# Performance work log

Hardware: AMD Instinct MI355X
Metric: run time of the kernel (lower is better)

## Reference

```python
import jax, jax.numpy as jnp
import numpy as np

H = 64; W = 64; P = 16; NPH = 4; NPW = 4; PH = 16; PW = 16; ZD = 32; HD = 1024; UD = 3; B = 256


def affine_grid(theta, Ho, Wo):
    # torch F.affine_grid, align_corners=False. theta [N,2,3] -> grid [N,Ho,Wo,2]
    xs = (2.0 * jnp.arange(Wo, dtype=theta.dtype) + 1.0) / Wo - 1.0
    ys = (2.0 * jnp.arange(Ho, dtype=theta.dtype) + 1.0) / Ho - 1.0
    X, Y = jnp.meshgrid(xs, ys)  # [Ho,Wo] each, x varies along last axis
    base = jnp.stack([X, Y, jnp.ones_like(X)], axis=-1)  # [Ho,Wo,3]
    return jnp.einsum('nij,hwj->nhwi', theta, base)


def grid_sample(img, grid):
    # torch F.grid_sample bilinear, padding_mode='zeros', align_corners=False
    # img [N,H,W], grid [N,Ho,Wo,2] in [-1,1]
    Hi, Wi = img.shape[1], img.shape[2]
    x = (grid[..., 0] + 1.0) * Wi / 2.0 - 0.5
    y = (grid[..., 1] + 1.0) * Hi / 2.0 - 0.5
    x0 = jnp.floor(x); y0 = jnp.floor(y)
    wx = x - x0; wy = y - y0

    def gather(ix, iy):
        valid = (ix >= 0) & (ix < Wi) & (iy >= 0) & (iy < Hi)
        ixc = jnp.clip(ix, 0, Wi - 1).astype(jnp.int32)
        iyc = jnp.clip(iy, 0, Hi - 1).astype(jnp.int32)
        v = jax.vmap(lambda im, yy, xx: im[yy, xx])(img, iyc, ixc)
        return jnp.where(valid, v, 0.0)

    return (gather(x0, y0) * (1 - wx) * (1 - wy)
            + gather(x0 + 1, y0) * wx * (1 - wy)
            + gather(x0, y0 + 1) * (1 - wx) * wy
            + gather(x0 + 1, y0 + 1) * wx * wy)


def rot_tr(u):
    # rotTrMatrix: u [N,3] (angle, tx, ty) -> [N,2,3]
    c = jnp.cos(u[:, 0]); s = jnp.sin(u[:, 0])
    R = jnp.stack([jnp.stack([c, -s], -1), jnp.stack([s, c], -1)], -2)  # [N,2,2]
    return jnp.concatenate([R, u[:, 1:3, None]], axis=2)


def anchor_theta():
    # anchor_move: identity rotation + per-part grid-cell-center translations
    tx = (np.arange(NPW) * (W / NPW) + W / NPW / 2) / W - 0.5
    ty = (np.arange(NPH) * (H / NPH) + H / NPH / 2) / H - 0.5
    th = np.tile(np.concatenate([np.eye(2), np.zeros((2, 1))], axis=1)[None], (P, 1, 1)).astype(np.float32)
    for k in range(P):
        th[k, 0, 2] = tx[k % NPW]
        th[k, 1, 2] = ty[k // NPW]
    return jnp.asarray(th)


def forward(inputs, W1, b1, W2, b2, Wum, bum, Wuv, buv, Wgm, bgm, Wgv, bgv, Wz, M, eps_u, eps_g):
    hid = jax.nn.relu(inputs.reshape(-1, H * W) @ W1 + b1)
    hid = jax.nn.relu(hid @ W2 + b2)
    # global transform distribution (note: F.threshold(x,-6,6) -> 6 where x<=-6)
    gmu = jnp.tanh(hid @ Wgm + bgm)
    gpre = hid @ Wgv + bgv
    gvar = jnp.exp(jnp.where(gpre > -6.0, gpre, 6.0))
    gu = gmu + gvar * eps_g  # sample_u uses mu + var*eps (var, not std) as in source
    # per-part transform distribution (F.threshold(x,-6,-6) -> clamp below at -6)
    umu = jnp.tanh(hid @ Wum + bum)
    upre = hid @ Wuv + buv
    uvar = jnp.exp(jnp.where(upre > -6.0, upre, -6.0))
    u = (umu + uvar * eps_u).reshape(-1, UD)  # [B*P,3]
    # decode parts (input is ones, as in source)
    parts = jax.nn.sigmoid(jnp.ones((B, ZD), inputs.dtype) @ Wz).reshape(B * P, PH, PW)
    padh = (H - PH) // 2; padw = (W - PW) // 2
    parts = jnp.pad(parts, ((0, 0), (padh, H - PH - padh), (padw, W - PW - padw)))
    # anchor placement of parts and kernel masks
    th_a = jnp.tile(anchor_theta(), (B, 1, 1))  # [B*P,2,3], part-minor ordering
    g_a = affine_grid(th_a, H, W)
    parts = grid_sample(parts, g_a)                     # [B*P,H,W]
    KM = grid_sample(M[:B * P].reshape(B * P, H, W), g_a)
    # per-part rotation+translation for parts; translation-only for kernel
    theta = rot_tr(u)                                   # [B*P,2,3]
    g = affine_grid(theta, H, W)
    eye = jnp.broadcast_to(jnp.eye(2, dtype=theta.dtype), (B * P, 2, 2))
    theta_K = jnp.concatenate([eye, theta[:, :, 2:3]], axis=2)
    g_K = affine_grid(theta_K, H, W)
    KM = grid_sample(KM, g_K).reshape(B, P, H, W)
    xp = grid_sample(parts, g).reshape(B, P, H, W)
    # masked weighted compositing
    num = jnp.sum(xp * KM, axis=1)
    den = jnp.sum(KM, axis=1)
    den = jnp.where(den == 0.0, 1.0, den)
    x = num / den
    # global transform
    theta_g = rot_tr(gu)
    g_g = affine_grid(theta_g, H, W)
    return grid_sample(x, g_g)[:, None]  # [B,1,H,W]


def setup_inputs() -> dict:
    key = jax.random.key(0)
    ks = jax.random.split(key, 18)

    def lin(k, fin, fout):
        return jax.random.normal(k, (fin, fout), jnp.float32) / np.sqrt(fin)

    return {
        'inputs': jax.random.uniform(ks[0], (B, H * W), jnp.float32),
        'W1': lin(ks[1], H * W, HD), 'b1': jnp.zeros((HD,), jnp.float32),
        'W2': lin(ks[2], HD, HD), 'b2': jnp.zeros((HD,), jnp.float32),
        'Wum': lin(ks[3], HD, P * UD), 'bum': jnp.zeros((P * UD,), jnp.float32),
        'Wuv': lin(ks[4], HD, P * UD), 'buv': jnp.zeros((P * UD,), jnp.float32),
        'Wgm': lin(ks[5], HD, UD), 'bgm': jnp.zeros((UD,), jnp.float32),
        'Wgv': lin(ks[6], HD, UD), 'bgv': jnp.zeros((UD,), jnp.float32),
        'Wz': lin(ks[7], ZD, P * PH * PW),
        'M': jax.random.uniform(ks[8], (B * P, 1, H, W), jnp.float32),
        'eps_u': jax.random.normal(ks[9], (B, P * UD), jnp.float32),
        'eps_g': jax.random.normal(ks[10], (B, UD), jnp.float32),
    }


def reference(inputs, W1, b1, W2, b2, Wum, bum, Wuv, buv, Wgm, bgm, Wgv, bgv, Wz, M, eps_u, eps_g):
    return forward(inputs, W1, b1, W2, b2, Wum, bum, Wuv, buv, Wgm, bgm, Wgv, bgv, Wz, M, eps_u, eps_g)
```

## Files before the change

kernel.cpp:

```cpp
#include <hip/hip_runtime.h>
#include <math.h>

#define SPLITK 8

typedef __bf16 bf16x8 __attribute__((ext_vector_type(8)));
typedef float  f32x4  __attribute__((ext_vector_type(4)));

__device__ inline unsigned short bf16rne(float x) {
    unsigned int u = __float_as_uint(x);
    unsigned int r = u + 0x7FFFu + ((u >> 16) & 1u);
    return (unsigned short)(r >> 16);
}
__device__ inline float bf16tof(unsigned short h) {
    return __uint_as_float(((unsigned int)h) << 16);
}

__global__ __launch_bounds__(256) void prep_all(
    const float* __restrict__ inputs,
    const float* __restrict__ W1, const float* __restrict__ W2,
    const float* __restrict__ Wum, const float* __restrict__ Wuv,
    const float* __restrict__ Wgm, const float* __restrict__ Wgv,
    const float* __restrict__ Wz,
    unsigned short* __restrict__ Ahi, unsigned short* __restrict__ Alo,
    unsigned short* __restrict__ W1Thi, unsigned short* __restrict__ W1Tlo,
    unsigned short* __restrict__ W2Thi, unsigned short* __restrict__ W2Tlo,
    float* __restrict__ WT, float* __restrict__ partsb)
{
    __shared__ float t[32][33];
    int bid = blockIdx.x;
    int tid = threadIdx.x;
    if (bid < 4096 || (bid >= 8192 && bid < 9216)) {
        const float* W = (bid < 4096) ? W1 : W2;
        unsigned short* Thi = (bid < 4096) ? W1Thi : W2Thi;
        unsigned short* Tlo = (bid < 4096) ? W1Tlo : W2Tlo;
        int K = (bid < 4096) ? 4096 : 1024;
        int b2 = (bid < 4096) ? bid : (bid - 8192);
        int n0 = (b2 & 31) * 32, k0 = (b2 >> 5) * 32;
        int c = tid & 31, r0 = tid >> 5;
#pragma unroll
        for (int i = 0; i < 4; i++)
            t[r0 + 8 * i][c] = W[(size_t)(k0 + r0 + 8 * i) * 1024 + n0 + c];
        __syncthreads();
        int kk = tid & 31, n1 = tid >> 5;
#pragma unroll
        for (int i = 0; i < 4; i++) {
            float x = t[kk][n1 + 8 * i];
            unsigned short h = bf16rne(x);
            unsigned short l = bf16rne(x - bf16tof(h));
            size_t o = (size_t)(n0 + n1 + 8 * i) * K + k0 + kk;
            Thi[o] = h;
            Tlo[o] = l;
        }
    } else if (bid < 8192) {
        int id = (bid - 4096) * 256 + tid;
        float x = inputs[id];
        unsigned short h = bf16rne(x);
        Ahi[id] = h;
        Alo[id] = bf16rne(x - bf16tof(h));
    } else if (bid < 9624) {
        int id = (bid - 9216) * 256 + tid;
        int o = id >> 10;
        int k = id & 1023;
        float v;
        if (o < 48)       v = Wum[k * 48 + o];
        else if (o < 96)  v = Wuv[k * 48 + (o - 48)];
        else if (o < 99)  v = Wgm[k * 3 + (o - 96)];
        else              v = Wgv[k * 3 + (o - 99)];
        WT[id] = v;
    } else {
        int idx = (bid - 9624) * 256 + tid;
        float s = 0.f;
#pragma unroll
        for (int z = 0; z < 32; z++) s += Wz[z * 4096 + idx];
        partsb[idx] = 1.f / (1.f + expf(-s));
    }
}

__global__ __launch_bounds__(256) void gemm_bf16x3(
    const unsigned short* __restrict__ Ahi, const unsigned short* __restrict__ Alo,
    const unsigned short* __restrict__ Bhi, const unsigned short* __restrict__ Blo,
    float* __restrict__ psum, int K, int kchunk)
{
    __shared__ unsigned short Ah[4096], Al[4096], Bh[4096], Bl[4096];
    int tid = threadIdx.x;
    int n0 = blockIdx.x * 64, m0 = blockIdx.y * 64;
    int kb = blockIdx.z * kchunk;
    int wid = tid >> 6, lane = tid & 63;
    int wm = wid & 1, wn = wid >> 1;
    int lm = lane & 15, q = lane >> 4;

    int r0 = tid >> 3, ch0 = tid & 7;
    int r1 = (tid + 256) >> 3, ch1 = (tid + 256) & 7;
    int l0 = r0 * 64 + 8 * (ch0 ^ (r0 & 7));
    int l1 = r1 * 64 + 8 * (ch1 ^ (r1 & 7));
    size_t ga0 = (size_t)(m0 + r0) * K + kb + ch0 * 8;
    size_t ga1 = (size_t)(m0 + r1) * K + kb + ch1 * 8;
    size_t gb0 = (size_t)(n0 + r0) * K + kb + ch0 * 8;
    size_t gb1 = (size_t)(n0 + r1) * K + kb + ch1 * 8;

    f32x4 acc[2][2] = {};

    int nkt = kchunk >> 6;
    uint4 vah0, vah1, val0, val1, vbh0, vbh1, vbl0, vbl1;
    vah0 = *(const uint4*)(Ahi + ga0);
    vah1 = *(const uint4*)(Ahi + ga1);
    val0 = *(const uint4*)(Alo + ga0);
    val1 = *(const uint4*)(Alo + ga1);
    vbh0 = *(const uint4*)(Bhi + gb0);
    vbh1 = *(const uint4*)(Bhi + gb1);
    vbl0 = *(const uint4*)(Blo + gb0);
    vbl1 = *(const uint4*)(Blo + gb1);

    int frm0 = (wm * 32 + lm) * 64;
    int frm1 = (wm * 32 + 16 + lm) * 64;
    int frn0 = (wn * 32 + lm) * 64;
    int frn1 = (wn * 32 + 16 + lm) * 64;
    int sw = lm & 7;

    for (int kt = 0; kt < nkt; kt++) {
        __syncthreads();
        *(uint4*)(Ah + l0) = vah0;
        *(uint4*)(Ah + l1) = vah1;
        *(uint4*)(Al + l0) = val0;
        *(uint4*)(Al + l1) = val1;
        *(uint4*)(Bh + l0) = vbh0;
        *(uint4*)(Bh + l1) = vbh1;
        *(uint4*)(Bl + l0) = vbl0;
        *(uint4*)(Bl + l1) = vbl1;
        __syncthreads();
        if (kt + 1 < nkt) {
            size_t o = (size_t)(kt + 1) * 64;
            vah0 = *(const uint4*)(Ahi + ga0 + o);
            vah1 = *(const uint4*)(Ahi + ga1 + o);
            val0 = *(const uint4*)(Alo + ga0 + o);
            val1 = *(const uint4*)(Alo + ga1 + o);
            vbh0 = *(const uint4*)(Bhi + gb0 + o);
            vbh1 = *(const uint4*)(Bhi + gb1 + o);
            vbl0 = *(const uint4*)(Blo + gb0 + o);
            vbl1 = *(const uint4*)(Blo + gb1 + o);
        }
#pragma unroll
        for (int ks = 0; ks < 2; ks++) {
            int cidx = 8 * (((ks << 2) + q) ^ sw);
            bf16x8 ah0 = *(const bf16x8*)(Ah + frm0 + cidx);
            bf16x8 ah1 = *(const bf16x8*)(Ah + frm1 + cidx);
            bf16x8 al0 = *(const bf16x8*)(Al + frm0 + cidx);
            bf16x8 al1 = *(const bf16x8*)(Al + frm1 + cidx);
            bf16x8 bh0 = *(const bf16x8*)(Bh + frn0 + cidx);
            bf16x8 bh1 = *(const bf16x8*)(Bh + frn1 + cidx);
            bf16x8 bl0 = *(const bf16x8*)(Bl + frn0 + cidx);
            bf16x8 bl1 = *(const bf16x8*)(Bl + frn1 + cidx);
            acc[0][0] = __builtin_amdgcn_mfma_f32_16x16x32_bf16(ah0, bh0, acc[0][0], 0, 0, 0);
            acc[0][0] = __builtin_amdgcn_mfma_f32_16x16x32_bf16(ah0, bl0, acc[0][0], 0, 0, 0);
            acc[0][0] = __builtin_amdgcn_mfma_f32_16x16x32_bf16(al0, bh0, acc[0][0], 0, 0, 0);
            acc[0][1] = __builtin_amdgcn_mfma_f32_16x16x32_bf16(ah0, bh1, acc[0][1], 0, 0, 0);
            acc[0][1] = __builtin_amdgcn_mfma_f32_16x16x32_bf16(ah0, bl1, acc[0][1], 0, 0, 0);
            acc[0][1] = __builtin_amdgcn_mfma_f32_16x16x32_bf16(al0, bh1, acc[0][1], 0, 0, 0);
            acc[1][0] = __builtin_amdgcn_mfma_f32_16x16x32_bf16(ah1, bh0, acc[1][0], 0, 0, 0);
            acc[1][0] = __builtin_amdgcn_mfma_f32_16x16x32_bf16(ah1, bl0, acc[1][0], 0, 0, 0);
            acc[1][0] = __builtin_amdgcn_mfma_f32_16x16x32_bf16(al1, bh0, acc[1][0], 0, 0, 0);
            acc[1][1] = __builtin_amdgcn_mfma_f32_16x16x32_bf16(ah1, bh1, acc[1][1], 0, 0, 0);
            acc[1][1] = __builtin_amdgcn_mfma_f32_16x16x32_bf16(ah1, bl1, acc[1][1], 0, 0, 0);
            acc[1][1] = __builtin_amdgcn_mfma_f32_16x16x32_bf16(al1, bh1, acc[1][1], 0, 0, 0);
        }
    }

    float* op = psum + (size_t)blockIdx.z * (256 * 1024);
#pragma unroll
    for (int mt = 0; mt < 2; mt++)
#pragma unroll
        for (int nt = 0; nt < 2; nt++) {
            int row = m0 + wm * 32 + mt * 16 + q * 4;
            int col = n0 + wn * 32 + nt * 16 + lm;
#pragma unroll
            for (int r = 0; r < 4; r++)
                op[(size_t)(row + r) * 1024 + col] = acc[mt][nt][r];
        }
}

__global__ __launch_bounds__(256) void reduce_bias_relu_split(
    const float* __restrict__ psum, const float* __restrict__ bias,
    unsigned short* __restrict__ hi, unsigned short* __restrict__ lo)
{
    int i = blockIdx.x * 256 + threadIdx.x;
    float v = 0.f;
#pragma unroll
    for (int s = 0; s < SPLITK; s++) v += psum[(size_t)s * 262144 + i];
    v += bias[i & 1023];
    v = fmaxf(v, 0.f);
    unsigned short h = bf16rne(v);
    hi[i] = h;
    lo[i] = bf16rne(v - bf16tof(h));
}

__global__ __launch_bounds__(512) void heads_v3(
    const float* __restrict__ psum, const float* __restrict__ b2,
    const float* __restrict__ WT,
    const float* __restrict__ bum, const float* __restrict__ buv,
    const float* __restrict__ bgm, const float* __restrict__ bgv,
    const float* __restrict__ eps_u, const float* __restrict__ eps_g,
    float* __restrict__ u_out, float* __restrict__ gu_out)
{
    int b = blockIdx.x;
    int tid = threadIdx.x;
    int w = tid >> 6, l = tid & 63;

    float4 hr[4];
#pragma unroll
    for (int i = 0; i < 4; i++) {
        int k = b * 1024 + i * 256 + l * 4;
        float4 acc = *(const float4*)(psum + k);
#pragma unroll
        for (int s = 1; s < SPLITK; s++) {
            float4 t = *(const float4*)(psum + (size_t)s * 262144 + k);
            acc.x += t.x; acc.y += t.y; acc.z += t.z; acc.w += t.w;
        }
        float4 bb = *(const float4*)(b2 + i * 256 + l * 4);
        acc.x = fmaxf(acc.x + bb.x, 0.f);
        acc.y = fmaxf(acc.y + bb.y, 0.f);
        acc.z = fmaxf(acc.z + bb.z, 0.f);
        acc.w = fmaxf(acc.w + bb.w, 0.f);
        hr[i] = acc;
    }

    int o = w;
    int rm = (o < 48) ? o : (48 + o);
    int rv = (o < 48) ? (o + 48) : (51 + o);
    float4 wm[4], wv[4];
    {
        const float* wp = WT + rm * 1024 + l * 4;
#pragma unroll
        for (int i = 0; i < 4; i++) wm[i] = *(const float4*)(wp + i * 256);
        wp = WT + rv * 1024 + l * 4;
#pragma unroll
        for (int i = 0; i < 4; i++) wv[i] = *(const float4*)(wp + i * 256);
    }

    while (o < 51) {
        int onext = o + 8;
        float4 wmn[4], wvn[4];
        if (onext < 51) {
            int rm2 = (onext < 48) ? onext : (48 + onext);
            int rv2 = (onext < 48) ? (onext + 48) : (51 + onext);
            const float* wp = WT + rm2 * 1024 + l * 4;
#pragma unroll
            for (int i = 0; i < 4; i++) wmn[i] = *(const float4*)(wp + i * 256);
            wp = WT + rv2 * 1024 + l * 4;
#pragma unroll
            for (int i = 0; i < 4; i++) wvn[i] = *(const float4*)(wp + i * 256);
        }
        float am = 0.f, av = 0.f;
#pragma unroll
        for (int i = 0; i < 4; i++) {
            am = fmaf(hr[i].x, wm[i].x, am);
            am = fmaf(hr[i].y, wm[i].y, am);
            am = fmaf(hr[i].z, wm[i].z, am);
            am = fmaf(hr[i].w, wm[i].w, am);
            av = fmaf(hr[i].x, wv[i].x, av);
            av = fmaf(hr[i].y, wv[i].y, av);
            av = fmaf(hr[i].z, wv[i].z, av);
            av = fmaf(hr[i].w, wv[i].w, av);
        }
#pragma unroll
        for (int s = 32; s; s >>= 1) {
            am += __shfl_xor(am, s, 64);
            av += __shfl_xor(av, s, 64);
        }
        if (l == 0) {
            if (o < 48) {
                float umu = tanhf(am + bum[o]);
                float uvar = expf(fmaxf(av + buv[o], -6.f));
                u_out[b * 48 + o] = umu + uvar * eps_u[b * 48 + o];
            } else {
                int n = o - 48;
                float gmu = tanhf(am + bgm[n]);
                float gpre = av + bgv[n];
                float gvar = expf(gpre > -6.f ? gpre : 6.f);
                gu_out[b * 3 + n] = gmu + gvar * eps_g[b * 3 + n];
            }
        }
#pragma unroll
        for (int i = 0; i < 4; i++) { wm[i] = wmn[i]; wv[i] = wvn[i]; }
        o = onext;
    }
}

__global__ __launch_bounds__(256) void composite_v6b(
    const float* __restrict__ M, const float* __restrict__ parts,
    const float* __restrict__ u, float* __restrict__ xout)
{
    __shared__ float patch[4096];
    __shared__ float plane[2][17 * 64];
    __shared__ float pc[16], psn[16], ptx[16], pty[16];
    int b = blockIdx.x >> 2;
    int quarter = blockIdx.x & 3;
    int tid = threadIdx.x;
    int brow0 = quarter * 16;

    for (int i = tid; i < 4096; i += 256) patch[i] = parts[i];
    if (tid < 16) {
        const float* up = u + (b * 16 + tid) * 3;
        float ang = up[0];
        pc[tid] = cosf(ang);
        psn[tid] = sinf(ang);
        ptx[tid] = up[1];
        pty[tid] = up[2];
    }
    __syncthreads();

    int j = tid & 63;
    int i0 = brow0 + (tid >> 6) * 4;
    float xnv = (float)(2 * j + 1) * (1.f / 64.f) - 1.f;

    float num[4] = {}, den[4] = {};
    const float* Mb = M + ((size_t)(b * 16) << 12);

    auto calc_iy = [&](int p, int& iy, int& iY, float& wy) {
        int dy = 8 * (p >> 2) - 12;
        float ay = fminf(fmaxf(32.f * pty[p], -16384.f), 16384.f);
        float fay = floorf(ay);
        wy = ay - fay;
        iy = (int)fay;
        iY = iy + dy;
    };

    int rr0 = tid >> 4, c0 = tid & 15;
    int rr1 = (tid + 256) >> 4, c1 = (tid + 256) & 15;

    int iy_arr[17], iY_arr[17]; float wy_arr[17];
#pragma unroll
    for (int p = 0; p < 16; p++) calc_iy(p, iy_arr[p], iY_arr[p], wy_arr[p]);

    float4 pfA0, pfA1;
    {
        int lo = brow0 + iY_arr[0];
        pfA0 = *(const float4*)(Mb + (min(max(lo + rr0, 0), 63) << 6) + c0 * 4);
        if (tid < 16)
            pfA1 = *(const float4*)(Mb + (min(max(lo + rr1, 0), 63) << 6) + c1 * 4);
        float4* dst = (float4*)plane[0];
        dst[tid] = pfA0;
        if (tid < 16) dst[tid + 256] = pfA1;
    }
    {
        int lo = brow0 + iY_arr[1];
        const float* Mp = Mb + (1 << 12);
        pfA0 = *(const float4*)(Mp + (min(max(lo + rr0, 0), 63) << 6) + c0 * 4);
        if (tid < 16)
            pfA1 = *(const float4*)(Mp + (min(max(lo + rr1, 0), 63) << 6) + c1 * 4);
    }
    __syncthreads();

    for (int p = 0; p < 16; p++) {
        int cur = p & 1;
        if (p + 1 < 16) {
            float4* dst = (float4*)plane[1 - cur];
            dst[tid] = pfA0;
            if (tid < 16) dst[tid + 256] = pfA1;
        }
        if (p + 2 < 16) {
            int lo = brow0 + iY_arr[p + 2];
            const float* Mp = Mb + ((size_t)(p + 2) << 12);
            pfA0 = *(const float4*)(Mp + (min(max(lo + rr0, 0), 63) << 6) + c0 * 4);
            if (tid < 16)
                pfA1 = *(const float4*)(Mp + (min(max(lo + rr1, 0), 63) << 6) + c1 * 4);
        }

        int iy = iy_arr[p], iY = iY_arr[p];
        float wy = wy_arr[p];
        int dx = 8 * (p & 3) - 12;
        int dy = 8 * (p >> 2) - 12;
        float c = pc[p], s = psn[p], tx = ptx[p];

        float ax = fminf(fmaxf(32.f * tx, -16384.f), 16384.f);
        float fax = floorf(ax);
        float wx = ax - fax;
        int ix = (int)fax;

        int x0 = j + ix;
        int X = x0 + dx;
        bool vc0 = ((unsigned)x0 < 64u) && ((unsigned)X < 64u);
        bool vc1 = ((unsigned)(x0 + 1) < 64u) && ((unsigned)(X + 1) < 64u);
        float w0 = vc0 ? (1.f - wx) : 0.f;
        float w1 = vc1 ? wx : 0.f;
        int Xc0 = min(max(X, 0), 63);
        int Xc1 = min(max(X + 1, 0), 63);

        const float* pl = plane[cur];
        float R[5];
#pragma unroll
        for (int r = 0; r < 5; r++) {
            int i = i0 + r;
            bool vr = ((unsigned)(i + iy) < 64u) && ((unsigned)(i + iY) < 64u);
            int lrow = (tid >> 6) * 4 + r;
            const float* row = pl + (lrow << 6);
            float val = fmaf(w0, row[Xc0], w1 * row[Xc1]);
            R[r] = vr ? val : 0.f;
        }

        float Ax = fmaf(c, xnv, tx);
        float Ay = fmaf(s, xnv, pty[p]);
        int ox = 24 - dx, oy = 24 - dy;
        float oxf = (float)ox, oyf = (float)oy;
        const float* pp = patch + (p << 8);
#pragma unroll
        for (int r = 0; r < 4; r++) {
            int i = i0 + r;
            float km = fmaf(wy, R[r + 1] - R[r], R[r]);
            den[r] += km;

            float ynv = (float)(2 * i + 1) * (1.f / 64.f) - 1.f;
            float gx = fmaf(-s, ynv, Ax);
            float gy = fmaf(c, ynv, Ay);
            float xs = fmaf(gx, 32.f, 31.5f);
            float ysv = fmaf(gy, 32.f, 31.5f);
            if (xs >= oxf - 1.f && xs < oxf + 16.f &&
                ysv >= oyf - 1.f && ysv < oyf + 16.f) {
                float xf = floorf(xs), yf = floorf(ysv);
                float wxx = xs - xf, wyy = ysv - yf;
                int a0 = (int)yf - oy;
                int b0c = (int)xf - ox;
                float v00 = 0.f, v10 = 0.f, v01 = 0.f, v11 = 0.f;
                if ((unsigned)a0 < 16u) {
                    const float* pr = pp + a0 * 16;
                    if ((unsigned)b0c < 16u) v00 = pr[b0c];
                    if ((unsigned)(b0c + 1) < 16u) v10 = pr[b0c + 1];
                }
                if ((unsigned)(a0 + 1) < 16u) {
                    const float* pr = pp + (a0 + 1) * 16;
                    if ((unsigned)b0c < 16u) v01 = pr[b0c];
                    if ((unsigned)(b0c + 1) < 16u) v11 = pr[b0c + 1];
                }
                float top = fmaf(wxx, v10 - v00, v00);
                float bot = fmaf(wxx, v11 - v01, v01);
                float xp = fmaf(wyy, bot - top, top);
                num[r] = fmaf(xp, km, num[r]);
            }
        }
        __syncthreads();
    }

    float* xo = xout + ((size_t)b << 12);
#pragma unroll
    for (int r = 0; r < 4; r++) {
        float d = (den[r] == 0.f) ? 1.f : den[r];
        xo[(i0 + r) * 64 + j] = num[r] / d;
    }
}

__global__ __launch_bounds__(256) void final_kernel(
    const float* __restrict__ xin, const float* __restrict__ gu,
    float* __restrict__ out)
{
    int id = blockIdx.x * 256 + threadIdx.x;
    int b = id >> 12;
    int pix = id & 4095;
    int ii = pix >> 6, jj = pix & 63;
    float ang = gu[b * 3 + 0], tx = gu[b * 3 + 1], ty = gu[b * 3 + 2];
    float c = cosf(ang), s = sinf(ang);
    float xn = (float)(2 * jj + 1) * (1.f / 64.f) - 1.f;
    float yn = (float)(2 * ii + 1) * (1.f / 64.f) - 1.f;
    float gx = c * xn - s * yn + tx;
    float gy = s * xn + c * yn + ty;
    float xs = (gx + 1.f) * 32.f - 0.5f;
    float ysv = (gy + 1.f) * 32.f - 0.5f;
    float xf = floorf(xs), yf = floorf(ysv);
    float wx = xs - xf, wy = ysv - yf;
    int x0 = (int)xf, y0 = (int)yf;
    const float* xp = xin + ((size_t)b << 12);
    float v00 = 0.f, v10 = 0.f, v01 = 0.f, v11 = 0.f;
    bool vx0 = (unsigned)x0 < 64u, vx1 = (unsigned)(x0 + 1) < 64u;
    if ((unsigned)y0 < 64u) {
        if (vx0) v00 = xp[y0 * 64 + x0];
        if (vx1) v10 = xp[y0 * 64 + x0 + 1];
    }
    if ((unsigned)(y0 + 1) < 64u) {
        if (vx0) v01 = xp[(y0 + 1) * 64 + x0];
        if (vx1) v11 = xp[(y0 + 1) * 64 + x0 + 1];
    }
    out[id] = v00 * (1.f - wx) * (1.f - wy) + v10 * wx * (1.f - wy)
            + v01 * (1.f - wx) * wy + v11 * wx * wy;
}

extern "C" void kernel_launch(void* const* d_in, const int* in_sizes, int n_in,
                              void* d_out, int out_size, void* d_ws, size_t ws_size,
                              hipStream_t stream)
{
    (void)in_sizes; (void)n_in; (void)out_size; (void)ws_size;
    const float* inputs = (const float*)d_in[0];
    const float* W1  = (const float*)d_in[1];
    const float* b1  = (const float*)d_in[2];
    const float* W2  = (const float*)d_in[3];
    const float* b2  = (const float*)d_in[4];
    const float* Wum = (const float*)d_in[5];
    const float* bum = (const float*)d_in[6];
    const float* Wuv = (const float*)d_in[7];
    const float* buv = (const float*)d_in[8];
    const float* Wgm = (const float*)d_in[9];
    const float* bgm = (const float*)d_in[10];
    const float* Wgv = (const float*)d_in[11];
    const float* bgv = (const float*)d_in[12];
    const float* Wz  = (const float*)d_in[13];
    const float* Mm  = (const float*)d_in[14];
    const float* eps_u = (const float*)d_in[15];
    const float* eps_g = (const float*)d_in[16];

    float* ws = (float*)d_ws;
    float* psum      = ws;
    float* x_buf     = ws + 2097152;
    float* u_buf     = ws + 3145728;
    float* gu_buf    = ws + 3158016;
    float* parts_buf = ws + 3158784;
    float* WTh_buf   = ws + 3162880;
    unsigned short* us = (unsigned short*)(ws + 3267328);
    unsigned short* Ahi   = us;
    unsigned short* Alo   = Ahi + 1048576;
    unsigned short* W1Thi = Alo + 1048576;
    unsigned short* W1Tlo = W1Thi + 4194304;
    unsigned short* W2Thi = W1Tlo + 4194304;
    unsigned short* W2Tlo = W2Thi + 1048576;
    unsigned short* H1hi  = W2Tlo + 1048576;
    unsigned short* H1lo  = H1hi + 262144;

    prep_all<<<9640, 256, 0, stream>>>(inputs, W1, W2, Wum, Wuv, Wgm, Wgv, Wz,
                                       Ahi, Alo, W1Thi, W1Tlo, W2Thi, W2Tlo,
                                       WTh_buf, parts_buf);

    gemm_bf16x3<<<dim3(16, 4, SPLITK), 256, 0, stream>>>(Ahi, Alo, W1Thi, W1Tlo,
                                                         psum, 4096, 4096 / SPLITK);
    reduce_bias_relu_split<<<1024, 256, 0, stream>>>(psum, b1, H1hi, H1lo);
    gemm_bf16x3<<<dim3(16, 4, SPLITK), 256, 0, stream>>>(H1hi, H1lo, W2Thi, W2Tlo,
                                                         psum, 1024, 1024 / SPLITK);
    heads_v3<<<256, 512, 0, stream>>>(psum, b2, WTh_buf, bum, buv, bgm, bgv,
                                      eps_u, eps_g, u_buf, gu_buf);
    composite_v6b<<<1024, 256, 0, stream>>>(Mm, parts_buf, u_buf, x_buf);
    final_kernel<<<4096, 256, 0, stream>>>(x_buf, gu_buf, (float*)d_out);
}
```

Before: 207.7 us.

## Fuse split-K reduction into GEMM1 and composite with final warp

The first GEMM now uses a per-tile atomic counter, so the last split-K block for each tile sums the partials and applies bias, ReLU and the bf16 hi/lo split. This removes the separate reduction kernel. The composite and final grid-sample kernels are merged into one 1024-thread block per batch image, which loads whole 64x64 M planes into shared memory and warps the composited image from shared memory instead of going through a global buffer. The trade-off is fewer blocks (256) with larger shared-memory use, plus a threadfence/atomic serialization tail in the GEMM.

```diff
diff --git a/kernel.cpp b/kernel.cpp
--- a/kernel.cpp
+++ b/kernel.cpp
@@ -24,7 +24,7 @@
     unsigned short* __restrict__ Ahi, unsigned short* __restrict__ Alo,
     unsigned short* __restrict__ W1Thi, unsigned short* __restrict__ W1Tlo,
     unsigned short* __restrict__ W2Thi, unsigned short* __restrict__ W2Tlo,
-    float* __restrict__ WT, float* __restrict__ partsb)
+    float* __restrict__ WT, float* __restrict__ partsb, int* __restrict__ ctr)
 {
     __shared__ float t[32][33];
     int bid = blockIdx.x;
@@ -73,15 +73,20 @@
 #pragma unroll
         for (int z = 0; z < 32; z++) s += Wz[z * 4096 + idx];
         partsb[idx] = 1.f / (1.f + expf(-s));
-    }
-}
-
-__global__ __launch_bounds__(256) void gemm_bf16x3(
+        if (bid == 9639 && tid < 64) ctr[tid] = 0;
+    }
+}
+
+__global__ __launch_bounds__(256) void gemm_bf16x3_l1(
     const unsigned short* __restrict__ Ahi, const unsigned short* __restrict__ Alo,
     const unsigned short* __restrict__ Bhi, const unsigned short* __restrict__ Blo,
-    float* __restrict__ psum, int K, int kchunk)
+    float* __restrict__ psum, const float* __restrict__ b1,
+    unsigned short* __restrict__ H1hi, unsigned short* __restrict__ H1lo,
+    int* __restrict__ ctr)
 {
+    const int K = 4096, kchunk = 512;
     __shared__ unsigned short Ah[4096], Al[4096], Bh[4096], Bl[4096];
+    __shared__ int lastFlag;
     int tid = threadIdx.x;
     int n0 = blockIdx.x * 64, m0 = blockIdx.y * 64;
     int kb = blockIdx.z * kchunk;
@@ -176,21 +181,138 @@
             for (int r = 0; r < 4; r++)
                 op[(size_t)(row + r) * 1024 + col] = acc[mt][nt][r];
         }
-}
-
-__global__ __launch_bounds__(256) void reduce_bias_relu_split(
-    const float* __restrict__ psum, const float* __restrict__ bias,
-    unsigned short* __restrict__ hi, unsigned short* __restrict__ lo)
+
+    __syncthreads();
+    if (tid == 0) {
+        __threadfence();
+        int old = atomicAdd(&ctr[blockIdx.y * 16 + blockIdx.x], 1);
+        lastFlag = (old == SPLITK - 1);
+    }
+    __syncthreads();
+    if (!lastFlag) return;
+    __threadfence();
+
+#pragma unroll
+    for (int mt = 0; mt < 2; mt++)
+#pragma unroll
+        for (int nt = 0; nt < 2; nt++) {
+            int row = m0 + wm * 32 + mt * 16 + q * 4;
+            int col = n0 + wn * 32 + nt * 16 + lm;
+#pragma unroll
+            for (int r = 0; r < 4; r++) {
+                size_t e = (size_t)(row + r) * 1024 + col;
+                float v = 0.f;
+#pragma unroll
+                for (int s = 0; s < SPLITK; s++) v += psum[(size_t)s * 262144 + e];
+                v += b1[col];
+                v = fmaxf(v, 0.f);
+                unsigned short h = bf16rne(v);
+                H1hi[e] = h;
+                H1lo[e] = bf16rne(v - bf16tof(h));
+            }
+        }
+}
+
+__global__ __launch_bounds__(256) void gemm_bf16x3(
+    const unsigned short* __restrict__ Ahi, const unsigned short* __restrict__ Alo,
+    const unsigned short* __restrict__ Bhi, const unsigned short* __restrict__ Blo,
+    float* __restrict__ psum, int K, int kchunk)
 {
-    int i = blockIdx.x * 256 + threadIdx.x;
-    float v = 0.f;
-#pragma unroll
-    for (int s = 0; s < SPLITK; s++) v += psum[(size_t)s * 262144 + i];
-    v += bias[i & 1023];
-    v = fmaxf(v, 0.f);
-    unsigned short h = bf16rne(v);
-    hi[i] = h;
-    lo[i] = bf16rne(v - bf16tof(h));
+    __shared__ unsigned short Ah[4096], Al[4096], Bh[4096], Bl[4096];
+    int tid = threadIdx.x;
+    int n0 = blockIdx.x * 64, m0 = blockIdx.y * 64;
+    int kb = blockIdx.z * kchunk;
+    int wid = tid >> 6, lane = tid & 63;
+    int wm = wid & 1, wn = wid >> 1;
+    int lm = lane & 15, q = lane >> 4;
+
+    int r0 = tid >> 3, ch0 = tid & 7;
+    int r1 = (tid + 256) >> 3, ch1 = (tid + 256) & 7;
+    int l0 = r0 * 64 + 8 * (ch0 ^ (r0 & 7));
+    int l1 = r1 * 64 + 8 * (ch1 ^ (r1 & 7));
+    size_t ga0 = (size_t)(m0 + r0) * K + kb + ch0 * 8;
+    size_t ga1 = (size_t)(m0 + r1) * K + kb + ch1 * 8;
+    size_t gb0 = (size_t)(n0 + r0) * K + kb + ch0 * 8;
+    size_t gb1 = (size_t)(n0 + r1) * K + kb + ch1 * 8;
+
+    f32x4 acc[2][2] = {};
+
+    int nkt = kchunk >> 6;
+    uint4 vah0, vah1, val0, val1, vbh0, vbh1, vbl0, vbl1;
+    vah0 = *(const uint4*)(Ahi + ga0);
+    vah1 = *(const uint4*)(Ahi + ga1);
+    val0 = *(const uint4*)(Alo + ga0);
+    val1 = *(const uint4*)(Alo + ga1);
+    vbh0 = *(const uint4*)(Bhi + gb0);
+    vbh1 = *(const uint4*)(Bhi + gb1);
+    vbl0 = *(const uint4*)(Blo + gb0);
+    vbl1 = *(const uint4*)(Blo + gb1);
+
+    int frm0 = (wm * 32 + lm) * 64;
+    int frm1 = (wm * 32 + 16 + lm) * 64;
+    int frn0 = (wn * 32 + lm) * 64;
+    int frn1 = (wn * 32 + 16 + lm) * 64;
+    int sw = lm & 7;
+
+    for (int kt = 0; kt < nkt; kt++) {
+        __syncthreads();
+        *(uint4*)(Ah + l0) = vah0;
+        *(uint4*)(Ah + l1) = vah1;
+        *(uint4*)(Al + l0) = val0;
+        *(uint4*)(Al + l1) = val1;
+        *(uint4*)(Bh + l0) = vbh0;
+        *(uint4*)(Bh + l1) = vbh1;
+        *(uint4*)(Bl + l0) = vbl0;
+        *(uint4*)(Bl + l1) = vbl1;
+        __syncthreads();
+        if (kt + 1 < nkt) {
+            size_t o = (size_t)(kt + 1) * 64;
+            vah0 = *(const uint4*)(Ahi + ga0 + o);
+            vah1 = *(const uint4*)(Ahi + ga1 + o);
+            val0 = *(const uint4*)(Alo + ga0 + o);
+            val1 = *(const uint4*)(Alo + ga1 + o);
+            vbh0 = *(const uint4*)(Bhi + gb0 + o);
+            vbh1 = *(const uint4*)(Bhi + gb1 + o);
+            vbl0 = *(const uint4*)(Blo + gb0 + o);
+            vbl1 = *(const uint4*)(Blo + gb1 + o);
+        }
+#pragma unroll
+        for (int ks = 0; ks < 2; ks++) {
+            int cidx = 8 * (((ks << 2) + q) ^ sw);
+            bf16x8 ah0 = *(const bf16x8*)(Ah + frm0 + cidx);
+            bf16x8 ah1 = *(const bf16x8*)(Ah + frm1 + cidx);
+            bf16x8 al0 = *(const bf16x8*)(Al + frm0 + cidx);
+            bf16x8 al1 = *(const bf16x8*)(Al + frm1 + cidx);
+            bf16x8 bh0 = *(const bf16x8*)(Bh + frn0 + cidx);
+            bf16x8 bh1 = *(const bf16x8*)(Bh + frn1 + cidx);
+            bf16x8 bl0 = *(const bf16x8*)(Bl + frn0 + cidx);
+            bf16x8 bl1 = *(const bf16x8*)(Bl + frn1 + cidx);
+            acc[0][0] = __builtin_amdgcn_mfma_f32_16x16x32_bf16(ah0, bh0, acc[0][0], 0, 0, 0);
+            acc[0][0] = __builtin_amdgcn_mfma_f32_16x16x32_bf16(ah0, bl0, acc[0][0], 0, 0, 0);
+            acc[0][0] = __builtin_amdgcn_mfma_f32_16x16x32_bf16(al0, bh0, acc[0][0], 0, 0, 0);
+            acc[0][1] = __builtin_amdgcn_mfma_f32_16x16x32_bf16(ah0, bh1, acc[0][1], 0, 0, 0);
+            acc[0][1] = __builtin_amdgcn_mfma_f32_16x16x32_bf16(ah0, bl1, acc[0][1], 0, 0, 0);
+            acc[0][1] = __builtin_amdgcn_mfma_f32_16x16x32_bf16(al0, bh1, acc[0][1], 0, 0, 0);
+            acc[1][0] = __builtin_amdgcn_mfma_f32_16x16x32_bf16(ah1, bh0, acc[1][0], 0, 0, 0);
+            acc[1][0] = __builtin_amdgcn_mfma_f32_16x16x32_bf16(ah1, bl0, acc[1][0], 0, 0, 0);
+            acc[1][0] = __builtin_amdgcn_mfma_f32_16x16x32_bf16(al1, bh0, acc[1][0], 0, 0, 0);
+            acc[1][1] = __builtin_amdgcn_mfma_f32_16x16x32_bf16(ah1, bh1, acc[1][1], 0, 0, 0);
+            acc[1][1] = __builtin_amdgcn_mfma_f32_16x16x32_bf16(ah1, bl1, acc[1][1], 0, 0, 0);
+            acc[1][1] = __builtin_amdgcn_mfma_f32_16x16x32_bf16(al1, bh1, acc[1][1], 0, 0, 0);
+        }
+    }
+
+    float* op = psum + (size_t)blockIdx.z * (256 * 1024);
+#pragma unroll
+    for (int mt = 0; mt < 2; mt++)
+#pragma unroll
+        for (int nt = 0; nt < 2; nt++) {
+            int row = m0 + wm * 32 + mt * 16 + q * 4;
+            int col = n0 + wn * 32 + nt * 16 + lm;
+#pragma unroll
+            for (int r = 0; r < 4; r++)
+                op[(size_t)(row + r) * 1024 + col] = acc[mt][nt][r];
+        }
 }
 
 __global__ __launch_bounds__(512) void heads_v3(
@@ -285,19 +407,18 @@
     }
 }
 
-__global__ __launch_bounds__(256) void composite_v6b(
+__global__ __launch_bounds__(1024) void composite_final(
     const float* __restrict__ M, const float* __restrict__ parts,
-    const float* __restrict__ u, float* __restrict__ xout)
+    const float* __restrict__ u, const float* __restrict__ gu,
+    float* __restrict__ out)
 {
     __shared__ float patch[4096];
-    __shared__ float plane[2][17 * 64];
+    __shared__ float plane[2][4096];
     __shared__ float pc[16], psn[16], ptx[16], pty[16];
-    int b = blockIdx.x >> 2;
-    int quarter = blockIdx.x & 3;
+    int b = blockIdx.x;
     int tid = threadIdx.x;
-    int brow0 = quarter * 16;
-
-    for (int i = tid; i < 4096; i += 256) patch[i] = parts[i];
+
+    for (int i = tid; i < 4096; i += 1024) patch[i] = parts[i];
     if (tid < 16) {
         const float* up = u + (b * 16 + tid) * 3;
         float ang = up[0];
@@ -306,75 +427,36 @@
         ptx[tid] = up[1];
         pty[tid] = up[2];
     }
+
+    const float* Mb = M + ((size_t)(b * 16) << 12);
+    ((float4*)plane[0])[tid] = ((const float4*)Mb)[tid];
+    float4 pfn = ((const float4*)(Mb + 4096))[tid];
     __syncthreads();
 
     int j = tid & 63;
-    int i0 = brow0 + (tid >> 6) * 4;
+    int i0 = (tid >> 6) * 4;
     float xnv = (float)(2 * j + 1) * (1.f / 64.f) - 1.f;
 
     float num[4] = {}, den[4] = {};
-    const float* Mb = M + ((size_t)(b * 16) << 12);
-
-    auto calc_iy = [&](int p, int& iy, int& iY, float& wy) {
-        int dy = 8 * (p >> 2) - 12;
-        float ay = fminf(fmaxf(32.f * pty[p], -16384.f), 16384.f);
-        float fay = floorf(ay);
-        wy = ay - fay;
-        iy = (int)fay;
-        iY = iy + dy;
-    };
-
-    int rr0 = tid >> 4, c0 = tid & 15;
-    int rr1 = (tid + 256) >> 4, c1 = (tid + 256) & 15;
-
-    int iy_arr[17], iY_arr[17]; float wy_arr[17];
-#pragma unroll
-    for (int p = 0; p < 16; p++) calc_iy(p, iy_arr[p], iY_arr[p], wy_arr[p]);
-
-    float4 pfA0, pfA1;
-    {
-        int lo = brow0 + iY_arr[0];
-        pfA0 = *(const float4*)(Mb + (min(max(lo + rr0, 0), 63) << 6) + c0 * 4);
-        if (tid < 16)
-            pfA1 = *(const float4*)(Mb + (min(max(lo + rr1, 0), 63) << 6) + c1 * 4);
-        float4* dst = (float4*)plane[0];
-        dst[tid] = pfA0;
-        if (tid < 16) dst[tid + 256] = pfA1;
-    }
-    {
-        int lo = brow0 + iY_arr[1];
-        const float* Mp = Mb + (1 << 12);
-        pfA0 = *(const float4*)(Mp + (min(max(lo + rr0, 0), 63) << 6) + c0 * 4);
-        if (tid < 16)
-            pfA1 = *(const float4*)(Mp + (min(max(lo + rr1, 0), 63) << 6) + c1 * 4);
-    }
-    __syncthreads();
 
     for (int p = 0; p < 16; p++) {
         int cur = p & 1;
-        if (p + 1 < 16) {
-            float4* dst = (float4*)plane[1 - cur];
-            dst[tid] = pfA0;
-            if (tid < 16) dst[tid + 256] = pfA1;
-        }
-        if (p + 2 < 16) {
-            int lo = brow0 + iY_arr[p + 2];
-            const float* Mp = Mb + ((size_t)(p + 2) << 12);
-            pfA0 = *(const float4*)(Mp + (min(max(lo + rr0, 0), 63) << 6) + c0 * 4);
-            if (tid < 16)
-                pfA1 = *(const float4*)(Mp + (min(max(lo + rr1, 0), 63) << 6) + c1 * 4);
-        }
-
-        int iy = iy_arr[p], iY = iY_arr[p];
-        float wy = wy_arr[p];
+        if (p + 1 < 16) ((float4*)plane[1 - cur])[tid] = pfn;
+        if (p + 2 < 16) pfn = ((const float4*)(Mb + ((size_t)(p + 2) << 12)))[tid];
+
         int dx = 8 * (p & 3) - 12;
         int dy = 8 * (p >> 2) - 12;
-        float c = pc[p], s = psn[p], tx = ptx[p];
+        float c = pc[p], s = psn[p], tx = ptx[p], ty = pty[p];
 
         float ax = fminf(fmaxf(32.f * tx, -16384.f), 16384.f);
         float fax = floorf(ax);
         float wx = ax - fax;
         int ix = (int)fax;
+        float ay = fminf(fmaxf(32.f * ty, -16384.f), 16384.f);
+        float fay = floorf(ay);
+        float wy = ay - fay;
+        int iy = (int)fay;
+        int iY = iy + dy;
 
         int x0 = j + ix;
         int X = x0 + dx;
@@ -390,15 +472,16 @@
 #pragma unroll
         for (int r = 0; r < 5; r++) {
             int i = i0 + r;
-            bool vr = ((unsigned)(i + iy) < 64u) && ((unsigned)(i + iY) < 64u);
-            int lrow = (tid >> 6) * 4 + r;
-            const float* row = pl + (lrow << 6);
+            int ri = i + iY;
+            bool vr = ((unsigned)(i + iy) < 64u) && ((unsigned)ri < 64u);
+            int ric = min(max(ri, 0), 63);
+            const float* row = pl + (ric << 6);
             float val = fmaf(w0, row[Xc0], w1 * row[Xc1]);
             R[r] = vr ? val : 0.f;
         }
 
         float Ax = fmaf(c, xnv, tx);
-        float Ay = fmaf(s, xnv, pty[p]);
+        float Ay = fmaf(s, xnv, ty);
         int ox = 24 - dx, oy = 24 - dy;
         float oxf = (float)ox, oyf = (float)oy;
         const float* pp = patch + (p << 8);
@@ -439,46 +522,46 @@
         __syncthreads();
     }
 
-    float* xo = xout + ((size_t)b << 12);
+    float* xl = plane[0];
 #pragma unroll
     for (int r = 0; r < 4; r++) {
         float d = (den[r] == 0.f) ? 1.f : den[r];
-        xo[(i0 + r) * 64 + j] = num[r] / d;
-    }
-}
-
-__global__ __launch_bounds__(256) void final_kernel(
-    const float* __restrict__ xin, const float* __restrict__ gu,
-    float* __restrict__ out)
-{
-    int id = blockIdx.x * 256 + threadIdx.x;
-    int b = id >> 12;
-    int pix = id & 4095;
-    int ii = pix >> 6, jj = pix & 63;
-    float ang = gu[b * 3 + 0], tx = gu[b * 3 + 1], ty = gu[b * 3 + 2];
-    float c = cosf(ang), s = sinf(ang);
-    float xn = (float)(2 * jj + 1) * (1.f / 64.f) - 1.f;
-    float yn = (float)(2 * ii + 1) * (1.f / 64.f) - 1.f;
-    float gx = c * xn - s * yn + tx;
-    float gy = s * xn + c * yn + ty;
-    float xs = (gx + 1.f) * 32.f - 0.5f;
-    float ysv = (gy + 1.f) * 32.f - 0.5f;
-    float xf = floorf(xs), yf = floorf(ysv);
-    float wx = xs - xf, wy = ysv - yf;
-    int x0 = (int)xf, y0 = (int)yf;
-    const float* xp = xin + ((size_t)b << 12);
-    float v00 = 0.f, v10 = 0.f, v01 = 0.f, v11 = 0.f;
-    bool vx0 = (unsigned)x0 < 64u, vx1 = (unsigned)(x0 + 1) < 64u;
-    if ((unsigned)y0 < 64u) {
-        if (vx0) v00 = xp[y0 * 64 + x0];
-        if (vx1) v10 = xp[y0 * 64 + x0 + 1];
-    }
-    if ((unsigned)(y0 + 1) < 64u) {
-        if (vx0) v01 = xp[(y0 + 1) * 64 + x0];
-        if (vx1) v11 = xp[(y0 + 1) * 64 + x0 + 1];
-    }
-    out[id] = v00 * (1.f - wx) * (1.f - wy) + v10 * wx * (1.f - wy)
-            + v01 * (1.f - wx) * wy + v11 * wx * wy;
+        xl[(i0 + r) * 64 + j] = num[r] / d;
+    }
+    __syncthreads();
+
+    float ang = gu[b * 3 + 0], gtx = gu[b * 3 + 1], gty = gu[b * 3 + 2];
+    float cg = cosf(ang), sg = sinf(ang);
+    float* ob = out + ((size_t)b << 12);
+#pragma unroll
+    for (int r = 0; r < 4; r++) {
+        int i = i0 + r;
+        float ynv = (float)(2 * i + 1) * (1.f / 64.f) - 1.f;
+        float gx = cg * xnv - sg * ynv + gtx;
+        float gy = sg * xnv + cg * ynv + gty;
+        gx = fminf(fmaxf(gx, -8.f), 8.f);
+        gy = fminf(fmaxf(gy, -8.f), 8.f);
+        float xs = fmaf(gx, 32.f, 31.5f);
+        float ysv = fmaf(gy, 32.f, 31.5f);
+        float xf = floorf(xs), yf = floorf(ysv);
+        float wx = xs - xf, wy = ysv - yf;
+        int x0 = (int)xf, y0 = (int)yf;
+        float v00 = 0.f, v10 = 0.f, v01 = 0.f, v11 = 0.f;
+        bool vx0 = (unsigned)x0 < 64u, vx1 = (unsigned)(x0 + 1) < 64u;
+        if ((unsigned)y0 < 64u) {
+            const float* row = xl + y0 * 64;
+            if (vx0) v00 = row[x0];
+            if (vx1) v10 = row[x0 + 1];
+        }
+        if ((unsigned)(y0 + 1) < 64u) {
+            const float* row = xl + (y0 + 1) * 64;
+            if (vx0) v01 = row[x0];
+            if (vx1) v11 = row[x0 + 1];
+        }
+        float top = fmaf(wx, v10 - v00, v00);
+        float bot = fmaf(wx, v11 - v01, v01);
+        ob[i * 64 + j] = fmaf(wy, bot - top, top);
+    }
 }
 
 extern "C" void kernel_launch(void* const* d_in, const int* in_sizes, int n_in,
@@ -506,12 +589,12 @@
 
     float* ws = (float*)d_ws;
     float* psum      = ws;
-    float* x_buf     = ws + 2097152;
-    float* u_buf     = ws + 3145728;
-    float* gu_buf    = ws + 3158016;
-    float* parts_buf = ws + 3158784;
-    float* WTh_buf   = ws + 3162880;
-    unsigned short* us = (unsigned short*)(ws + 3267328);
+    float* u_buf     = ws + 2097152;
+    float* gu_buf    = u_buf + 12288;
+    float* parts_buf = gu_buf + 768;
+    float* WTh_buf   = parts_buf + 4096;
+    int*   ctr       = (int*)(WTh_buf + 104448);
+    unsigned short* us = (unsigned short*)(ctr + 64);
     unsigned short* Ahi   = us;
     unsigned short* Alo   = Ahi + 1048576;
     unsigned short* W1Thi = Alo + 1048576;
@@ -523,15 +606,14 @@
 
     prep_all<<<9640, 256, 0, stream>>>(inputs, W1, W2, Wum, Wuv, Wgm, Wgv, Wz,
                                        Ahi, Alo, W1Thi, W1Tlo, W2Thi, W2Tlo,
-                                       WTh_buf, parts_buf);
-
-    gemm_bf16x3<<<dim3(16, 4, SPLITK), 256, 0, stream>>>(Ahi, Alo, W1Thi, W1Tlo,
-                                                         psum, 4096, 4096 / SPLITK);
-    reduce_bias_relu_split<<<1024, 256, 0, stream>>>(psum, b1, H1hi, H1lo);
+                                       WTh_buf, parts_buf, ctr);
+
+    gemm_bf16x3_l1<<<dim3(16, 4, SPLITK), 256, 0, stream>>>(
+        Ahi, Alo, W1Thi, W1Tlo, psum, b1, H1hi, H1lo, ctr);
     gemm_bf16x3<<<dim3(16, 4, SPLITK), 256, 0, stream>>>(H1hi, H1lo, W2Thi, W2Tlo,
                                                          psum, 1024, 1024 / SPLITK);
     heads_v3<<<256, 512, 0, stream>>>(psum, b2, WTh_buf, bum, buv, bgm, bgv,
                                       eps_u, eps_g, u_buf, gu_buf);
-    composite_v6b<<<1024, 256, 0, stream>>>(Mm, parts_buf, u_buf, x_buf);
-    final_kernel<<<4096, 256, 0, stream>>>(x_buf, gu_buf, (float*)d_out);
-}
+    composite_final<<<256, 1024, 0, stream>>>(Mm, parts_buf, u_buf, gu_buf,
+                                              (float*)d_out);
+}
```

New measurement: 221.7 us. 6.8% more time.

## Fuse composite and final grid-sample into one per-image 1024-thread kernel

Applied to the files above, without the earlier changes.

Merges the compositing kernel and the final affine grid_sample kernel. One 1024-thread block now handles a whole image, keeps the composited image in shared memory and samples it there, which removes the global round trip of x_buf and one launch. Each block now stages full 64x64 mask planes instead of shifted 17-row windows, and rows are clamped at read time. The trade is fewer blocks (256 instead of 1024), which lowers parallelism on a large GPU, and more shared memory per block. It also adds a clamp on grid coordinates.

```diff
diff --git a/kernel.cpp b/kernel.cpp
--- a/kernel.cpp
+++ b/kernel.cpp
@@ -285,19 +285,18 @@
     }
 }
 
-__global__ __launch_bounds__(256) void composite_v6b(
+__global__ __launch_bounds__(1024) void composite_final(
     const float* __restrict__ M, const float* __restrict__ parts,
-    const float* __restrict__ u, float* __restrict__ xout)
+    const float* __restrict__ u, const float* __restrict__ gu,
+    float* __restrict__ out)
 {
     __shared__ float patch[4096];
-    __shared__ float plane[2][17 * 64];
+    __shared__ float plane[2][4096];
     __shared__ float pc[16], psn[16], ptx[16], pty[16];
-    int b = blockIdx.x >> 2;
-    int quarter = blockIdx.x & 3;
+    int b = blockIdx.x;
     int tid = threadIdx.x;
-    int brow0 = quarter * 16;
-
-    for (int i = tid; i < 4096; i += 256) patch[i] = parts[i];
+
+    for (int i = tid; i < 4096; i += 1024) patch[i] = parts[i];
     if (tid < 16) {
         const float* up = u + (b * 16 + tid) * 3;
         float ang = up[0];
@@ -306,75 +305,36 @@
         ptx[tid] = up[1];
         pty[tid] = up[2];
     }
+
+    const float* Mb = M + ((size_t)(b * 16) << 12);
+    ((float4*)plane[0])[tid] = ((const float4*)Mb)[tid];
+    float4 pfn = ((const float4*)(Mb + 4096))[tid];
     __syncthreads();
 
     int j = tid & 63;
-    int i0 = brow0 + (tid >> 6) * 4;
+    int i0 = (tid >> 6) * 4;
     float xnv = (float)(2 * j + 1) * (1.f / 64.f) - 1.f;
 
     float num[4] = {}, den[4] = {};
-    const float* Mb = M + ((size_t)(b * 16) << 12);
-
-    auto calc_iy = [&](int p, int& iy, int& iY, float& wy) {
-        int dy = 8 * (p >> 2) - 12;
-        float ay = fminf(fmaxf(32.f * pty[p], -16384.f), 16384.f);
-        float fay = floorf(ay);
-        wy = ay - fay;
-        iy = (int)fay;
-        iY = iy + dy;
-    };
-
-    int rr0 = tid >> 4, c0 = tid & 15;
-    int rr1 = (tid + 256) >> 4, c1 = (tid + 256) & 15;
-
-    int iy_arr[17], iY_arr[17]; float wy_arr[17];
-#pragma unroll
-    for (int p = 0; p < 16; p++) calc_iy(p, iy_arr[p], iY_arr[p], wy_arr[p]);
-
-    float4 pfA0, pfA1;
-    {
-        int lo = brow0 + iY_arr[0];
-        pfA0 = *(const float4*)(Mb + (min(max(lo + rr0, 0), 63) << 6) + c0 * 4);
-        if (tid < 16)
-            pfA1 = *(const float4*)(Mb + (min(max(lo + rr1, 0), 63) << 6) + c1 * 4);
-        float4* dst = (float4*)plane[0];
-        dst[tid] = pfA0;
-        if (tid < 16) dst[tid + 256] = pfA1;
-    }
-    {
-        int lo = brow0 + iY_arr[1];
-        const float* Mp = Mb + (1 << 12);
-        pfA0 = *(const float4*)(Mp + (min(max(lo + rr0, 0), 63) << 6) + c0 * 4);
-        if (tid < 16)
-            pfA1 = *(const float4*)(Mp + (min(max(lo + rr1, 0), 63) << 6) + c1 * 4);
-    }
-    __syncthreads();
 
     for (int p = 0; p < 16; p++) {
         int cur = p & 1;
-        if (p + 1 < 16) {
-            float4* dst = (float4*)plane[1 - cur];
-            dst[tid] = pfA0;
-            if (tid < 16) dst[tid + 256] = pfA1;
-        }
-        if (p + 2 < 16) {
-            int lo = brow0 + iY_arr[p + 2];
-            const float* Mp = Mb + ((size_t)(p + 2) << 12);
-            pfA0 = *(const float4*)(Mp + (min(max(lo + rr0, 0), 63) << 6) + c0 * 4);
-            if (tid < 16)
-                pfA1 = *(const float4*)(Mp + (min(max(lo + rr1, 0), 63) << 6) + c1 * 4);
-        }
-
-        int iy = iy_arr[p], iY = iY_arr[p];
-        float wy = wy_arr[p];
+        if (p + 1 < 16) ((float4*)plane[1 - cur])[tid] = pfn;
+        if (p + 2 < 16) pfn = ((const float4*)(Mb + ((size_t)(p + 2) << 12)))[tid];
+
         int dx = 8 * (p & 3) - 12;
         int dy = 8 * (p >> 2) - 12;
-        float c = pc[p], s = psn[p], tx = ptx[p];
+        float c = pc[p], s = psn[p], tx = ptx[p], ty = pty[p];
 
         float ax = fminf(fmaxf(32.f * tx, -16384.f), 16384.f);
         float fax = floorf(ax);
         float wx = ax - fax;
         int ix = (int)fax;
+        float ay = fminf(fmaxf(32.f * ty, -16384.f), 16384.f);
+        float fay = floorf(ay);
+        float wy = ay - fay;
+        int iy = (int)fay;
+        int iY = iy + dy;
 
         int x0 = j + ix;
         int X = x0 + dx;
@@ -390,15 +350,16 @@
 #pragma unroll
         for (int r = 0; r < 5; r++) {
             int i = i0 + r;
-            bool vr = ((unsigned)(i + iy) < 64u) && ((unsigned)(i + iY) < 64u);
-            int lrow = (tid >> 6) * 4 + r;
-            const float* row = pl + (lrow << 6);
+            int ri = i + iY;
+            bool vr = ((unsigned)(i + iy) < 64u) && ((unsigned)ri < 64u);
+            int ric = min(max(ri, 0), 63);
+            const float* row = pl + (ric << 6);
             float val = fmaf(w0, row[Xc0], w1 * row[Xc1]);
             R[r] = vr ? val : 0.f;
         }
 
         float Ax = fmaf(c, xnv, tx);
-        float Ay = fmaf(s, xnv, pty[p]);
+        float Ay = fmaf(s, xnv, ty);
         int ox = 24 - dx, oy = 24 - dy;
         float oxf = (float)ox, oyf = (float)oy;
         const float* pp = patch + (p << 8);
@@ -439,46 +400,46 @@
         __syncthreads();
     }
 
-    float* xo = xout + ((size_t)b << 12);
+    float* xl = plane[0];
 #pragma unroll
     for (int r = 0; r < 4; r++) {
         float d = (den[r] == 0.f) ? 1.f : den[r];
-        xo[(i0 + r) * 64 + j] = num[r] / d;
-    }
-}
-
-__global__ __launch_bounds__(256) void final_kernel(
-    const float* __restrict__ xin, const float* __restrict__ gu,
-    float* __restrict__ out)
-{
-    int id = blockIdx.x * 256 + threadIdx.x;
-    int b = id >> 12;
-    int pix = id & 4095;
-    int ii = pix >> 6, jj = pix & 63;
-    float ang = gu[b * 3 + 0], tx = gu[b * 3 + 1], ty = gu[b * 3 + 2];
-    float c = cosf(ang), s = sinf(ang);
-    float xn = (float)(2 * jj + 1) * (1.f / 64.f) - 1.f;
-    float yn = (float)(2 * ii + 1) * (1.f / 64.f) - 1.f;
-    float gx = c * xn - s * yn + tx;
-    float gy = s * xn + c * yn + ty;
-    float xs = (gx + 1.f) * 32.f - 0.5f;
-    float ysv = (gy + 1.f) * 32.f - 0.5f;
-    float xf = floorf(xs), yf = floorf(ysv);
-    float wx = xs - xf, wy = ysv - yf;
-    int x0 = (int)xf, y0 = (int)yf;
-    const float* xp = xin + ((size_t)b << 12);
-    float v00 = 0.f, v10 = 0.f, v01 = 0.f, v11 = 0.f;
-    bool vx0 = (unsigned)x0 < 64u, vx1 = (unsigned)(x0 + 1) < 64u;
-    if ((unsigned)y0 < 64u) {
-        if (vx0) v00 = xp[y0 * 64 + x0];
-        if (vx1) v10 = xp[y0 * 64 + x0 + 1];
-    }
-    if ((unsigned)(y0 + 1) < 64u) {
-        if (vx0) v01 = xp[(y0 + 1) * 64 + x0];
-        if (vx1) v11 = xp[(y0 + 1) * 64 + x0 + 1];
-    }
-    out[id] = v00 * (1.f - wx) * (1.f - wy) + v10 * wx * (1.f - wy)
-            + v01 * (1.f - wx) * wy + v11 * wx * wy;
+        xl[(i0 + r) * 64 + j] = num[r] / d;
+    }
+    __syncthreads();
+
+    float ang = gu[b * 3 + 0], gtx = gu[b * 3 + 1], gty = gu[b * 3 + 2];
+    float cg = cosf(ang), sg = sinf(ang);
+    float* ob = out + ((size_t)b << 12);
+#pragma unroll
+    for (int r = 0; r < 4; r++) {
+        int i = i0 + r;
+        float ynv = (float)(2 * i + 1) * (1.f / 64.f) - 1.f;
+        float gx = cg * xnv - sg * ynv + gtx;
+        float gy = sg * xnv + cg * ynv + gty;
+        gx = fminf(fmaxf(gx, -8.f), 8.f);
+        gy = fminf(fmaxf(gy, -8.f), 8.f);
+        float xs = fmaf(gx, 32.f, 31.5f);
+        float ysv = fmaf(gy, 32.f, 31.5f);
+        float xf = floorf(xs), yf = floorf(ysv);
+        float wx = xs - xf, wy = ysv - yf;
+        int x0 = (int)xf, y0 = (int)yf;
+        float v00 = 0.f, v10 = 0.f, v01 = 0.f, v11 = 0.f;
+        bool vx0 = (unsigned)x0 < 64u, vx1 = (unsigned)(x0 + 1) < 64u;
+        if ((unsigned)y0 < 64u) {
+            const float* row = xl + y0 * 64;
+            if (vx0) v00 = row[x0];
+            if (vx1) v10 = row[x0 + 1];
+        }
+        if ((unsigned)(y0 + 1) < 64u) {
+            const float* row = xl + (y0 + 1) * 64;
+            if (vx0) v01 = row[x0];
+            if (vx1) v11 = row[x0 + 1];
+        }
+        float top = fmaf(wx, v10 - v00, v00);
+        float bot = fmaf(wx, v11 - v01, v01);
+        ob[i * 64 + j] = fmaf(wy, bot - top, top);
+    }
 }
 
 extern "C" void kernel_launch(void* const* d_in, const int* in_sizes, int n_in,
@@ -506,12 +467,11 @@
 
     float* ws = (float*)d_ws;
     float* psum      = ws;
-    float* x_buf     = ws + 2097152;
-    float* u_buf     = ws + 3145728;
-    float* gu_buf    = ws + 3158016;
-    float* parts_buf = ws + 3158784;
-    float* WTh_buf   = ws + 3162880;
-    unsigned short* us = (unsigned short*)(ws + 3267328);
+    float* u_buf     = ws + 2097152;
+    float* gu_buf    = u_buf + 12288;
+    float* parts_buf = gu_buf + 768;
+    float* WTh_buf   = parts_buf + 4096;
+    unsigned short* us = (unsigned short*)(WTh_buf + 104448);
     unsigned short* Ahi   = us;
     unsigned short* Alo   = Ahi + 1048576;
     unsigned short* W1Thi = Alo + 1048576;
@@ -532,6 +492,6 @@
                                                          psum, 1024, 1024 / SPLITK);
     heads_v3<<<256, 512, 0, stream>>>(psum, b2, WTh_buf, bum, buv, bgm, bgv,
                                       eps_u, eps_g, u_buf, gu_buf);
-    composite_v6b<<<1024, 256, 0, stream>>>(Mm, parts_buf, u_buf, x_buf);
-    final_kernel<<<4096, 256, 0, stream>>>(x_buf, gu_buf, (float*)d_out);
-}
+    composite_final<<<256, 1024, 0, stream>>>(Mm, parts_buf, u_buf, gu_buf,
+                                              (float*)d_out);
+}
```

New measurement: 198.5 us. 1.05x faster.
